# Kernel tuning notes

Measured on AMD Instinct MI355X. Metric: run time of the kernel, lower is better.

The kernel has to match this reference:

```python
import jax, jax.numpy as jnp
import numpy as np

B = 16384
D_VIS, D_LANG, D_STATE = 768, 768, 64
D = 256          # d_model
E = 4            # n_experts
K = 2            # top_k
D_IN = D_VIS + D_LANG + D_STATE
EPS = 1e-5


def layernorm(x, g, b):
    mu = x.mean(-1, keepdims=True)
    var = ((x - mu) ** 2).mean(-1, keepdims=True)
    return g * (x - mu) / jnp.sqrt(var + EPS) + b


def setup_inputs() -> dict:
    key = jax.random.key(0)
    ks = jax.random.split(key, 16)
    s = 0.02
    return {
        "vis": jax.random.normal(ks[0], (B, D_VIS), jnp.float32),
        "lang": jax.random.normal(ks[1], (B, D_LANG), jnp.float32),
        "state": jax.random.normal(ks[2], (B, D_STATE), jnp.float32),
        # fusion: Linear(d_in, d_model) + LayerNorm
        "Wf": jax.random.normal(ks[3], (D_IN, D), jnp.float32) * s,
        "bf": jnp.zeros((D,), jnp.float32),
        "gf": jnp.ones((D,), jnp.float32),
        "bfln": jnp.zeros((D,), jnp.float32),
        # gate (bias=False); random instead of zeros so routing is nontrivial
        "Wg": jax.random.normal(ks[4], (D, E), jnp.float32) * s,
        # stacked experts: Linear(d,2d) -> GELU -> Linear(2d,d) -> GELU -> Linear(d,d), then LN(x + net(x))
        "W1": jax.random.normal(ks[5], (E, D, 2 * D), jnp.float32) * s,
        "b1": jnp.zeros((E, 2 * D), jnp.float32),
        "W2": jax.random.normal(ks[6], (E, 2 * D, D), jnp.float32) * s,
        "b2": jnp.zeros((E, D), jnp.float32),
        "W3": jax.random.normal(ks[7], (E, D, D), jnp.float32) * s,
        "b3": jnp.zeros((E, D), jnp.float32),
        "eg": jnp.ones((E, D), jnp.float32),
        "eb": jnp.zeros((E, D), jnp.float32),
    }


def reference(vis, lang, state, Wf, bf, gf, bfln, Wg, W1, b1, W2, b2, W3, b3, eg, eb):
    gelu = lambda t: jax.nn.gelu(t, approximate=False)
    # fusion: Linear -> LayerNorm -> GELU  (dropout is eval-mode identity)
    x = jnp.concatenate([vis, lang, state], axis=-1) @ Wf + bf   # [B, D]
    x = gelu(layernorm(x, gf, bfln))

    logits = x @ Wg                                              # [B, E]
    all_probs = jax.nn.softmax(logits, axis=-1)
    top_vals, top_idx = jax.lax.top_k(logits, K)                 # [B, K]
    top_w = jax.nn.softmax(top_vals, axis=-1)                    # [B, K]

    # all experts densely (E small); original computes same math per masked subset
    h = gelu(jnp.einsum('bd,edh->beh', x, W1) + b1)              # [B, E, 2D]
    h = gelu(jnp.einsum('beh,ehd->bed', h, W2) + b2)             # [B, E, D]
    h = jnp.einsum('bed,edf->bef', h, W3) + b3                   # [B, E, D]
    y = layernorm(x[:, None, :] + h, eg, eb)                     # [B, E, D]

    # gather selected experts and combine with top-k weights
    y_sel = jnp.take_along_axis(y, top_idx[:, :, None], axis=1)  # [B, K, D]
    out = jnp.einsum('bk,bkd->bd', top_w, y_sel)                 # [B, D]

    # load-balance loss: importance x load
    counts = jnp.zeros((E,), x.dtype).at[top_idx.reshape(-1)].add(1.0)
    f_i = counts / (B * K)
    lb_loss = E * jnp.sum(f_i * all_probs.mean(0))
    return out, lb_loss
```

## Files before the change

kernel.cpp:

```cpp
#include <hip/hip_runtime.h>
#include <math.h>


typedef unsigned short u16;
typedef unsigned int u32;
typedef __attribute__((ext_vector_type(8))) short bf16x8;
typedef __attribute__((ext_vector_type(4))) float f32x4;

__device__ __forceinline__ float bf2f(u16 u) {
    union { u32 i; float f; } v; v.i = ((u32)u) << 16; return v.f;
}
__device__ __forceinline__ u16 f2bf(float f) {
    union { float f; u32 i; } v; v.f = f;
    u32 x = v.i;
    return (u16)((x + 0x7fffu + ((x >> 16) & 1u)) >> 16);
}
__device__ __forceinline__ float gelu_exact(float v) {
    return 0.5f * v * (1.0f + erff(v * 0.70710678118654752f));
}

typedef __attribute__((address_space(1))) void GV;
typedef __attribute__((address_space(3))) void SV;
__device__ __forceinline__ void gldlds(const void* g, void* l) {
    __builtin_amdgcn_global_load_lds((GV*)g, (SV*)l, 16, 0, 0);
}

__device__ __forceinline__ u32 pk2(u32 f0, u32 f1) {
    return __builtin_amdgcn_perm(f1, f0, 0x07060302);
}

__device__ __forceinline__ void stageA64_R32(const u16* Ag, int lda, u16* As, int tid) {
    int s = tid;
    int m = s >> 3, c = s & 7;
    gldlds(Ag + m * lda + (c ^ (m & 7)) * 8, As + s * 8);
}
__device__ __forceinline__ void stageB64(const u16* Bg, int ldb, u16* Bs, int tid) {
#pragma unroll
    for (int i = 0; i < 8; ++i) {
        int s = i * 256 + tid;
        int n = s >> 3, c = s & 7;
        gldlds(Bg + n * ldb + (c ^ (n & 7)) * 8, Bs + s * 8);
    }
}
__device__ __forceinline__ void compute64_R32(const u16* As, const u16* Bs, f32x4 acc[2][4],
                                              int w, int l16, int quad) {
#pragma unroll
    for (int ks = 0; ks < 2; ++ks) {
        bf16x8 a[2];
#pragma unroll
        for (int mt = 0; mt < 2; ++mt) {
            int m = mt * 16 + l16;
            a[mt] = *(const bf16x8*)(As + m * 64 + (((ks * 4 + quad) ^ (m & 7)) << 3));
        }
#pragma unroll
        for (int nt = 0; nt < 4; ++nt) {
            int n = w * 64 + nt * 16 + l16;
            bf16x8 b = *(const bf16x8*)(Bs + n * 64 + (((ks * 4 + quad) ^ (n & 7)) << 3));
#pragma unroll
            for (int mt = 0; mt < 2; ++mt)
                acc[mt][nt] = __builtin_amdgcn_mfma_f32_16x16x32_bf16(a[mt], b, acc[mt][nt], 0, 0, 0);
        }
    }
}
__device__ __forceinline__ void stageA128_512(const u16* Ag, int lda, u16* As, int tid) {
#pragma unroll
    for (int i = 0; i < 2; ++i) {
        int s = i * 512 + tid;
        int m = s >> 3, c = s & 7;
        gldlds(Ag + m * lda + (c ^ (m & 7)) * 8, As + s * 8);
    }
}
__device__ __forceinline__ void stageB64_512(const u16* Bg, int ldb, u16* Bs, int tid) {
#pragma unroll
    for (int i = 0; i < 4; ++i) {
        int s = i * 512 + tid;
        int n = s >> 3, c = s & 7;
        gldlds(Bg + n * ldb + (c ^ (n & 7)) * 8, Bs + s * 8);
    }
}
__device__ __forceinline__ void compute128_8w(const u16* As, const u16* Bs, f32x4 acc[4][4],
                                              int wrw, int wc, int l16, int quad) {
#pragma unroll
    for (int ks = 0; ks < 2; ++ks) {
        bf16x8 a[4];
#pragma unroll
        for (int mt = 0; mt < 4; ++mt) {
            int m = wrw * 64 + mt * 16 + l16;
            a[mt] = *(const bf16x8*)(As + m * 64 + (((ks * 4 + quad) ^ (m & 7)) << 3));
        }
#pragma unroll
        for (int nt = 0; nt < 4; ++nt) {
            int n = wc * 64 + nt * 16 + l16;
            bf16x8 b = *(const bf16x8*)(Bs + n * 64 + (((ks * 4 + quad) ^ (n & 7)) << 3));
#pragma unroll
            for (int mt = 0; mt < 4; ++mt)
                acc[mt][nt] = __builtin_amdgcn_mfma_f32_16x16x32_bf16(a[mt], b, acc[mt][nt], 0, 0, 0);
        }
    }
}

#define SEG_WF  409600
#define SEG_W1  524288
#define SEG_W2  524288
#define SEG_W3  262144
#define PREP_ITEMS (SEG_WF + SEG_W1 + SEG_W2 + SEG_W3 + 8)

__global__ __launch_bounds__(256) void prep_kernel(
    const float* __restrict__ Wf, const float* __restrict__ W1, const float* __restrict__ W2,
    const float* __restrict__ W3,
    u16* __restrict__ wft, u16* __restrict__ w1t, u16* __restrict__ w2t, u16* __restrict__ w3t,
    float* __restrict__ lbacc) {
    int idx = blockIdx.x * 256 + threadIdx.x;
    if (idx < SEG_WF) {
        int n = idx / 1600, k = idx % 1600;
        wft[idx] = f2bf(Wf[(size_t)k * 256 + n]);
        return;
    }
    idx -= SEG_WF;
    if (idx < SEG_W1) {
        int e = idx >> 17, r = idx & 131071;
        int n = r >> 8, k = r & 255;
        w1t[idx] = f2bf(W1[(size_t)e * 131072 + (size_t)k * 512 + n]);
        return;
    }
    idx -= SEG_W1;
    if (idx < SEG_W2) {
        int e = idx >> 17, r = idx & 131071;
        int n = r >> 9, k = r & 511;
        w2t[idx] = f2bf(W2[(size_t)e * 131072 + (size_t)k * 256 + n]);
        return;
    }
    idx -= SEG_W2;
    if (idx < SEG_W3) {
        int e = idx >> 16, r = idx & 65535;
        int n = r >> 8, k = r & 255;
        w3t[idx] = f2bf(W3[(size_t)e * 65536 + (size_t)k * 256 + n]);
        return;
    }
    idx -= SEG_W3;
    if (idx < 8) lbacc[idx] = 0.0f;
}

__global__ __launch_bounds__(512, 4) void fusion_kernel(
    const float* __restrict__ vis, const float* __restrict__ lang, const float* __restrict__ state,
    const u16* __restrict__ BT, const float* __restrict__ bfv_, const float* __restrict__ gf,
    const float* __restrict__ bfln, const float* __restrict__ Wg,
    u16* __restrict__ xbf, float* __restrict__ wr, float* __restrict__ lbacc) {
    __shared__ __align__(16) u32 Af[4096];
    __shared__ __align__(16) u16 Bs[16384];
    int tid = threadIdx.x;
    int w = tid >> 6, lane = tid & 63, quad = lane >> 4, l16 = lane & 15;
    int wrw = w >> 2, wc = w & 3;
    int m0 = blockIdx.x * 64;
    f32x4 acc[2][4] = {};

    for (int kit = 0; kit < 25; ++kit) {
        const float* base; int ld;
        if (kit < 12)      { base = vis   + (size_t)m0 * 768 + kit * 64;        ld = 768; }
        else if (kit < 24) { base = lang  + (size_t)m0 * 768 + (kit - 12) * 64; ld = 768; }
        else               { base = state + (size_t)m0 * 64;                    ld = 64; }
#pragma unroll
        for (int i = 0; i < 2; ++i) {
            int s = i * 512 + tid;
            int m = s >> 4, c = s & 15;
            gldlds(base + m * ld + (c ^ (m & 15)) * 4, Af + s * 4);
        }
        stageB64_512(BT + kit * 64, 1600, Bs, tid);
        __syncthreads();
#pragma unroll
        for (int ks = 0; ks < 2; ++ks) {
            bf16x8 a[2];
#pragma unroll
            for (int mt = 0; mt < 2; ++mt) {
                int m = wrw * 32 + mt * 16 + l16;
                int c0 = ks * 8 + quad * 2;
                const u32* rowp = Af + m * 64;
                uint4 f0 = *(const uint4*)(rowp + (c0 ^ (m & 15)) * 4);
                uint4 f1 = *(const uint4*)(rowp + ((c0 + 1) ^ (m & 15)) * 4);
                union { u32 u[4]; bf16x8 v; } pk;
                pk.u[0] = pk2(f0.x, f0.y); pk.u[1] = pk2(f0.z, f0.w);
                pk.u[2] = pk2(f1.x, f1.y); pk.u[3] = pk2(f1.z, f1.w);
                a[mt] = pk.v;
            }
#pragma unroll
            for (int nt = 0; nt < 4; ++nt) {
                int n = wc * 64 + nt * 16 + l16;
                bf16x8 b = *(const bf16x8*)(Bs + n * 64 + (((ks * 4 + quad) ^ (n & 7)) << 3));
#pragma unroll
                for (int mt = 0; mt < 2; ++mt)
                    acc[mt][nt] = __builtin_amdgcn_mfma_f32_16x16x32_bf16(a[mt], b, acc[mt][nt], 0, 0, 0);
            }
        }
        __syncthreads();
    }

    float2* red  = (float2*)Af;
    float*  muv  = (float*)(Af + 512);
    float*  rsv  = (float*)(Af + 576);
    float*  gred = (float*)(Af + 640);
    float*  sacc = (float*)(Af + 1664);

    float bv[4], gvv[4], blv[4]; float4 wgv[4];
#pragma unroll
    for (int nt = 0; nt < 4; ++nt) {
        int col = wc * 64 + nt * 16 + l16;
        bv[nt] = bfv_[col]; gvv[nt] = gf[col]; blv[nt] = bfln[col];
        wgv[nt] = *(const float4*)(Wg + col * 4);
    }
    if (tid < 8) sacc[tid] = 0.f;
#pragma unroll
    for (int mt = 0; mt < 2; ++mt)
#pragma unroll
        for (int r = 0; r < 4; ++r) {
            float ss = 0.f, qq = 0.f;
#pragma unroll
            for (int nt = 0; nt < 4; ++nt) {
                float v = acc[mt][nt][r] + bv[nt];
                acc[mt][nt][r] = v;
                ss += v; qq += v * v;
            }
#pragma unroll
            for (int d = 1; d < 16; d <<= 1) { ss += __shfl_xor(ss, d); qq += __shfl_xor(qq, d); }
            if (l16 == 0) red[w * 32 + mt * 16 + quad * 4 + r] = make_float2(ss, qq);
        }
    __syncthreads();
    if (tid < 64) {
        int wrh = tid >> 5, rl2 = tid & 31;
        float ss = 0.f, qq = 0.f;
#pragma unroll
        for (int ww = 0; ww < 4; ++ww) {
            float2 t = red[(wrh * 4 + ww) * 32 + rl2]; ss += t.x; qq += t.y;
        }
        float mu = ss * (1.f / 256.f);
        float var = qq * (1.f / 256.f) - mu * mu;
        muv[tid] = mu;
        rsv[tid] = 1.f / sqrtf(var + 1e-5f);
    }
    __syncthreads();
#pragma unroll
    for (int mt = 0; mt < 2; ++mt)
#pragma unroll
        for (int r = 0; r < 4; ++r) {
            int rl2 = mt * 16 + quad * 4 + r;
            int row = wrw * 32 + rl2;
            float mu = muv[row], rs = rsv[row];
#pragma unroll
            for (int nt = 0; nt < 4; ++nt) {
                int col = wc * 64 + nt * 16 + l16;
                float t = (acc[mt][nt][r] - mu) * rs * gvv[nt] + blv[nt];
                float g = gelu_exact(t);
                acc[mt][nt][r] = g;
                xbf[(size_t)(m0 + row) * 256 + col] = f2bf(g);
            }
        }
#pragma unroll
    for (int mt = 0; mt < 2; ++mt)
#pragma unroll
        for (int r = 0; r < 4; ++r) {
            int rl2 = mt * 16 + quad * 4 + r;
            float p0 = 0.f, p1 = 0.f, p2 = 0.f, p3 = 0.f;
#pragma unroll
            for (int nt = 0; nt < 4; ++nt) {
                float g = acc[mt][nt][r];
                p0 += g * wgv[nt].x; p1 += g * wgv[nt].y;
                p2 += g * wgv[nt].z; p3 += g * wgv[nt].w;
            }
#pragma unroll
            for (int d = 1; d < 16; d <<= 1) {
                p0 += __shfl_xor(p0, d); p1 += __shfl_xor(p1, d);
                p2 += __shfl_xor(p2, d); p3 += __shfl_xor(p3, d);
            }
            if (l16 == 0) {
                float* gp = gred + w * 128 + rl2 * 4;
                gp[0] = p0; gp[1] = p1; gp[2] = p2; gp[3] = p3;
            }
        }
    __syncthreads();
    if (tid < 64) {
        int row = tid, wrh = row >> 5, rl2 = row & 31;
        float lg[4];
#pragma unroll
        for (int e = 0; e < 4; ++e) {
            float s = 0.f;
#pragma unroll
            for (int ww = 0; ww < 4; ++ww) s += gred[(wrh * 4 + ww) * 128 + rl2 * 4 + e];
            lg[e] = s;
        }
        float mx = fmaxf(fmaxf(lg[0], lg[1]), fmaxf(lg[2], lg[3]));
        float ex[4]; float Z = 0.f;
#pragma unroll
        for (int e = 0; e < 4; ++e) { ex[e] = expf(lg[e] - mx); Z += ex[e]; }
        int i0 = 0; float v0 = lg[0];
#pragma unroll
        for (int e = 1; e < 4; ++e) if (lg[e] > v0) { v0 = lg[e]; i0 = e; }
        int i1 = -1; float v1 = -1e30f;
#pragma unroll
        for (int e = 0; e < 4; ++e) if (e != i0 && lg[e] > v1) { v1 = lg[e]; i1 = e; }
        float t = expf(v1 - v0);
        float wA = 1.f / (1.f + t), wB = t / (1.f + t);
        float w4[4] = {0.f, 0.f, 0.f, 0.f};
        w4[i0] = wA; w4[i1] = wB;
#pragma unroll
        for (int e = 0; e < 4; ++e) wr[(size_t)(m0 + row) * 4 + e] = w4[e];
#pragma unroll
        for (int e = 0; e < 4; ++e) atomicAdd(&sacc[e], ex[e] / Z);
        atomicAdd(&sacc[4 + i0], 1.f);
        atomicAdd(&sacc[4 + i1], 1.f);
    }
    __syncthreads();
    if (tid < 8) atomicAdd(lbacc + tid, sacc[tid]);
}

__global__ __launch_bounds__(512, 4) void expert_gemm_kernel(
    const u16* __restrict__ A, int lda, size_t aE,
    const u16* __restrict__ BT, size_t bE,
    const float* __restrict__ bias, int biasE,
    u16* __restrict__ outp, int ldo, size_t oE) {
    __shared__ __align__(16) u16 As[8192];
    __shared__ __align__(16) u16 Bs[16384];
    int tid = threadIdx.x;
    int w = tid >> 6, lane = tid & 63, quad = lane >> 4, l16 = lane & 15;
    int wrw = w >> 2, wc = w & 3;
    int m0 = blockIdx.x * 128;
    int col0 = blockIdx.y * 256;
    int e = blockIdx.z;
    f32x4 acc[4][4] = {};
    const u16* Ag = A + e * aE + (size_t)m0 * lda;
    const u16* Bg = BT + e * bE + (size_t)col0 * lda;
    int kiters = lda >> 6;
    for (int kit = 0; kit < kiters; ++kit) {
        stageA128_512(Ag + kit * 64, lda, As, tid);
        stageB64_512(Bg + kit * 64, lda, Bs, tid);
        __syncthreads();
        compute128_8w(As, Bs, acc, wrw, wc, l16, quad);
        __syncthreads();
    }
#pragma unroll
    for (int nt = 0; nt < 4; ++nt) {
        int col = col0 + wc * 64 + nt * 16 + l16;
        float bvv = bias[e * biasE + col];
#pragma unroll
        for (int mt = 0; mt < 4; ++mt)
#pragma unroll
            for (int r = 0; r < 4; ++r) {
                int row = m0 + wrw * 64 + mt * 16 + quad * 4 + r;
                outp[e * oE + (size_t)row * ldo + col] = f2bf(gelu_exact(acc[mt][nt][r] + bvv));
            }
    }
}

__global__ __launch_bounds__(256) void combine_kernel(
    const u16* __restrict__ h2, const u16* __restrict__ W3T,
    const float* __restrict__ b3, const float* __restrict__ eg, const float* __restrict__ eb,
    const u16* __restrict__ xbf, const float* __restrict__ wr,
    const float* __restrict__ lbacc, float* __restrict__ outp) {
    __shared__ __align__(16) u16 As[2048];
    __shared__ __align__(16) u16 Bs[16384];
    __shared__ __align__(16) u16 xs[8192];
    __shared__ float wl[128];
    int tid = threadIdx.x;
    int w = tid >> 6, lane = tid & 63, quad = lane >> 4, l16 = lane & 15;
    int m0 = blockIdx.x * 32;
    if (blockIdx.x == 0 && tid == 0) {
        float lb = 0.f;
#pragma unroll
        for (int e = 0; e < 4; ++e)
            lb += (lbacc[4 + e] / 32768.f) * (lbacc[e] / 16384.f);
        outp[4194304] = 4.f * lb;
    }
#pragma unroll
    for (int i = 0; i < 4; ++i) {
        int s = i * 256 + tid;
        *(uint4*)(xs + s * 8) = *(const uint4*)(xbf + (size_t)m0 * 256 + s * 8);
    }
    if (tid < 128) wl[tid] = wr[(size_t)m0 * 4 + tid];
    float2* red = (float2*)As;
    float* muv = (float*)((char*)As + 1024);
    float* rsv = (float*)((char*)As + 1152);
    f32x4 oacc[2][4] = {};
    for (int e = 0; e < 4; ++e) {
        __syncthreads();
        f32x4 acc[2][4] = {};
        const u16* Ag = h2 + ((size_t)e * 16384 + m0) * 256;
        const u16* Bg = W3T + (size_t)e * 65536;
        for (int kit = 0; kit < 4; ++kit) {
            stageA64_R32(Ag + kit * 64, 256, As, tid);
            stageB64(Bg + kit * 64, 256, Bs, tid);
            __syncthreads();
            compute64_R32(As, Bs, acc, w, l16, quad);
            __syncthreads();
        }
        float b3v[4], egv[4], ebv[4];
#pragma unroll
        for (int nt = 0; nt < 4; ++nt) {
            int col = w * 64 + nt * 16 + l16;
            b3v[nt] = b3[e * 256 + col]; egv[nt] = eg[e * 256 + col]; ebv[nt] = eb[e * 256 + col];
        }
#pragma unroll
        for (int mt = 0; mt < 2; ++mt)
#pragma unroll
            for (int r = 0; r < 4; ++r) {
                int rl = mt * 16 + quad * 4 + r;
                float ss = 0.f, qq = 0.f;
#pragma unroll
                for (int nt = 0; nt < 4; ++nt) {
                    int col = w * 64 + nt * 16 + l16;
                    float v = acc[mt][nt][r] + b3v[nt] + bf2f(xs[rl * 256 + col]);
                    acc[mt][nt][r] = v;
                    ss += v; qq += v * v;
                }
#pragma unroll
                for (int d = 1; d < 16; d <<= 1) { ss += __shfl_xor(ss, d); qq += __shfl_xor(qq, d); }
                if (l16 == 0) red[w * 32 + rl] = make_float2(ss, qq);
            }
        __syncthreads();
        if (tid < 32) {
            float ss = 0.f, qq = 0.f;
#pragma unroll
            for (int ww = 0; ww < 4; ++ww) { float2 t = red[ww * 32 + tid]; ss += t.x; qq += t.y; }
            float mu = ss * (1.f / 256.f);
            float var = qq * (1.f / 256.f) - mu * mu;
            muv[tid] = mu;
            rsv[tid] = 1.f / sqrtf(var + 1e-5f);
        }
        __syncthreads();
#pragma unroll
        for (int mt = 0; mt < 2; ++mt)
#pragma unroll
            for (int r = 0; r < 4; ++r) {
                int rl = mt * 16 + quad * 4 + r;
                float mu = muv[rl], rs = rsv[rl], we = wl[rl * 4 + e];
#pragma unroll
                for (int nt = 0; nt < 4; ++nt) {
                    float y = (acc[mt][nt][r] - mu) * rs * egv[nt] + ebv[nt];
                    oacc[mt][nt][r] += we * y;
                }
            }
    }
#pragma unroll
    for (int mt = 0; mt < 2; ++mt)
#pragma unroll
        for (int r = 0; r < 4; ++r) {
            int rl = mt * 16 + quad * 4 + r;
#pragma unroll
            for (int nt = 0; nt < 4; ++nt) {
                int col = w * 64 + nt * 16 + l16;
                outp[(size_t)(m0 + rl) * 256 + col] = oacc[mt][nt][r];
            }
        }
}

extern "C" void kernel_launch(void* const* d_in, const int* in_sizes, int n_in,
                              void* d_out, int out_size, void* d_ws, size_t ws_size,
                              hipStream_t stream) {
    const float* vis   = (const float*)d_in[0];
    const float* lang  = (const float*)d_in[1];
    const float* state = (const float*)d_in[2];
    const float* Wf    = (const float*)d_in[3];
    const float* bf_   = (const float*)d_in[4];
    const float* gf    = (const float*)d_in[5];
    const float* bfln  = (const float*)d_in[6];
    const float* Wg    = (const float*)d_in[7];
    const float* W1    = (const float*)d_in[8];
    const float* b1    = (const float*)d_in[9];
    const float* W2    = (const float*)d_in[10];
    const float* b2    = (const float*)d_in[11];
    const float* W3    = (const float*)d_in[12];
    const float* b3    = (const float*)d_in[13];
    const float* eg    = (const float*)d_in[14];
    const float* eb    = (const float*)d_in[15];
    float* outp = (float*)d_out;

    char* ws = (char*)d_ws;
    size_t off = 0;
    float* lbacc = (float*)(ws + off); off += 256;
    u16* WFT  = (u16*)(ws + off); off += 819200UL;
    u16* W1T  = (u16*)(ws + off); off += 1048576UL;
    u16* W2T  = (u16*)(ws + off); off += 1048576UL;
    u16* W3T  = (u16*)(ws + off); off += 524288UL;
    u16* XBF  = (u16*)(ws + off); off += 8388608UL;
    float* WR = (float*)(ws + off); off += 262144UL;
    u16* H1   = (u16*)(ws + off); off += 67108864UL;
    u16* H2   = (u16*)(ws + off); off += 33554432UL;
    if (ws_size < off) return;

    int prep_blocks = (PREP_ITEMS + 255) / 256;
    prep_kernel<<<prep_blocks, 256, 0, stream>>>(Wf, W1, W2, W3, WFT, W1T, W2T, W3T, lbacc);
    fusion_kernel<<<256, 512, 0, stream>>>(vis, lang, state, WFT, bf_, gf, bfln, Wg,
                                           XBF, WR, lbacc);
    expert_gemm_kernel<<<dim3(128, 2, 4), 512, 0, stream>>>(
        XBF, 256, 0, W1T, 131072, b1, 512, H1, 512, 8388608UL);
    expert_gemm_kernel<<<dim3(128, 1, 4), 512, 0, stream>>>(
        H1, 512, 8388608UL, W2T, 131072, b2, 256, H2, 256, 4194304UL);
    combine_kernel<<<512, 256, 0, stream>>>(H2, W3T, b3, eg, eb, XBF, WR, lbacc, outp);
}
```

Measured before the change: 319.1 us.

## Tile weight transpose via LDS, retile fusion and combine kernels

The prep kernel now transposes weights through a padded 32x32 shared-memory tile, so both the fp32 reads and the bf16 writes are coalesced instead of strided reads per element. The fusion kernel moves from 64-row to 32-row blocks with eight warps splitting the 256 columns, doubling the grid to 512 blocks for more parallelism. The combine kernel goes from 32-row to 64-row tiles, so each W3 tile staged in LDS is reused across twice as many rows. The trade-offs are more accumulator registers and LDS in combine, and in fusion the weight tile is reloaded for half as many rows per block.

```diff
diff --git a/kernel.cpp b/kernel.cpp
--- a/kernel.cpp
+++ b/kernel.cpp
@@ -29,10 +29,13 @@
     return __builtin_amdgcn_perm(f1, f0, 0x07060302);
 }
 
-__device__ __forceinline__ void stageA64_R32(const u16* Ag, int lda, u16* As, int tid) {
-    int s = tid;
-    int m = s >> 3, c = s & 7;
-    gldlds(Ag + m * lda + (c ^ (m & 7)) * 8, As + s * 8);
+__device__ __forceinline__ void stageA64(const u16* Ag, int lda, u16* As, int tid) {
+#pragma unroll
+    for (int i = 0; i < 2; ++i) {
+        int s = i * 256 + tid;
+        int m = s >> 3, c = s & 7;
+        gldlds(Ag + m * lda + (c ^ (m & 7)) * 8, As + s * 8);
+    }
 }
 __device__ __forceinline__ void stageB64(const u16* Bg, int ldb, u16* Bs, int tid) {
 #pragma unroll
@@ -42,13 +45,13 @@
         gldlds(Bg + n * ldb + (c ^ (n & 7)) * 8, Bs + s * 8);
     }
 }
-__device__ __forceinline__ void compute64_R32(const u16* As, const u16* Bs, f32x4 acc[2][4],
-                                              int w, int l16, int quad) {
+__device__ __forceinline__ void compute64(const u16* As, const u16* Bs, f32x4 acc[4][4],
+                                          int w, int l16, int quad) {
 #pragma unroll
     for (int ks = 0; ks < 2; ++ks) {
-        bf16x8 a[2];
-#pragma unroll
-        for (int mt = 0; mt < 2; ++mt) {
+        bf16x8 a[4];
+#pragma unroll
+        for (int mt = 0; mt < 4; ++mt) {
             int m = mt * 16 + l16;
             a[mt] = *(const bf16x8*)(As + m * 64 + (((ks * 4 + quad) ^ (m & 7)) << 3));
         }
@@ -57,7 +60,7 @@
             int n = w * 64 + nt * 16 + l16;
             bf16x8 b = *(const bf16x8*)(Bs + n * 64 + (((ks * 4 + quad) ^ (n & 7)) << 3));
 #pragma unroll
-            for (int mt = 0; mt < 2; ++mt)
+            for (int mt = 0; mt < 4; ++mt)
                 acc[mt][nt] = __builtin_amdgcn_mfma_f32_16x16x32_bf16(a[mt], b, acc[mt][nt], 0, 0, 0);
         }
     }
@@ -98,47 +101,36 @@
         }
     }
 }
-
-#define SEG_WF  409600
-#define SEG_W1  524288
-#define SEG_W2  524288
-#define SEG_W3  262144
-#define PREP_ITEMS (SEG_WF + SEG_W1 + SEG_W2 + SEG_W3 + 8)
 
 __global__ __launch_bounds__(256) void prep_kernel(
     const float* __restrict__ Wf, const float* __restrict__ W1, const float* __restrict__ W2,
     const float* __restrict__ W3,
     u16* __restrict__ wft, u16* __restrict__ w1t, u16* __restrict__ w2t, u16* __restrict__ w3t,
     float* __restrict__ lbacc) {
-    int idx = blockIdx.x * 256 + threadIdx.x;
-    if (idx < SEG_WF) {
-        int n = idx / 1600, k = idx % 1600;
-        wft[idx] = f2bf(Wf[(size_t)k * 256 + n]);
-        return;
-    }
-    idx -= SEG_WF;
-    if (idx < SEG_W1) {
-        int e = idx >> 17, r = idx & 131071;
-        int n = r >> 8, k = r & 255;
-        w1t[idx] = f2bf(W1[(size_t)e * 131072 + (size_t)k * 512 + n]);
-        return;
-    }
-    idx -= SEG_W1;
-    if (idx < SEG_W2) {
-        int e = idx >> 17, r = idx & 131071;
-        int n = r >> 9, k = r & 511;
-        w2t[idx] = f2bf(W2[(size_t)e * 131072 + (size_t)k * 256 + n]);
-        return;
-    }
-    idx -= SEG_W2;
-    if (idx < SEG_W3) {
-        int e = idx >> 16, r = idx & 65535;
-        int n = r >> 8, k = r & 255;
-        w3t[idx] = f2bf(W3[(size_t)e * 65536 + (size_t)k * 256 + n]);
-        return;
-    }
-    idx -= SEG_W3;
-    if (idx < 8) lbacc[idx] = 0.0f;
+    int b = blockIdx.x;
+    int tid = threadIdx.x;
+    const float* src; u16* dst; int K, N, kt, ntl;
+    if (b < 400)      { src = Wf; dst = wft; K = 1600; N = 256; kt = b % 50; ntl = b / 50; }
+    else if (b < 912) { int r = b - 400, e = r >> 7; r &= 127;
+                        src = W1 + (size_t)e * 131072; dst = w1t + (size_t)e * 131072;
+                        K = 256; N = 512; kt = r & 7; ntl = r >> 3; }
+    else if (b < 1424){ int r = b - 912, e = r >> 7; r &= 127;
+                        src = W2 + (size_t)e * 131072; dst = w2t + (size_t)e * 131072;
+                        K = 512; N = 256; kt = r & 15; ntl = r >> 4; }
+    else if (b < 1680){ int r = b - 1424, e = r >> 6; r &= 63;
+                        src = W3 + (size_t)e * 65536; dst = w3t + (size_t)e * 65536;
+                        K = 256; N = 256; kt = r & 7; ntl = r >> 3; }
+    else { if (tid < 8) lbacc[tid] = 0.0f; return; }
+    int k0 = kt * 32, n0 = ntl * 32;
+    __shared__ float tl[32][33];
+    int j = tid & 31, i0 = (tid >> 5) << 2;
+#pragma unroll
+    for (int ii = 0; ii < 4; ++ii)
+        tl[i0 + ii][j] = src[(size_t)(k0 + i0 + ii) * N + n0 + j];
+    __syncthreads();
+#pragma unroll
+    for (int ii = 0; ii < 4; ++ii)
+        dst[(size_t)(n0 + i0 + ii) * K + k0 + j] = f2bf(tl[j][i0 + ii]);
 }
 
 __global__ __launch_bounds__(512, 4) void fusion_kernel(
@@ -146,22 +138,20 @@
     const u16* __restrict__ BT, const float* __restrict__ bfv_, const float* __restrict__ gf,
     const float* __restrict__ bfln, const float* __restrict__ Wg,
     u16* __restrict__ xbf, float* __restrict__ wr, float* __restrict__ lbacc) {
-    __shared__ __align__(16) u32 Af[4096];
+    __shared__ __align__(16) u32 Af[2048];
     __shared__ __align__(16) u16 Bs[16384];
     int tid = threadIdx.x;
     int w = tid >> 6, lane = tid & 63, quad = lane >> 4, l16 = lane & 15;
-    int wrw = w >> 2, wc = w & 3;
-    int m0 = blockIdx.x * 64;
-    f32x4 acc[2][4] = {};
+    int m0 = blockIdx.x * 32;
+    f32x4 acc[2][2] = {};
 
     for (int kit = 0; kit < 25; ++kit) {
         const float* base; int ld;
         if (kit < 12)      { base = vis   + (size_t)m0 * 768 + kit * 64;        ld = 768; }
         else if (kit < 24) { base = lang  + (size_t)m0 * 768 + (kit - 12) * 64; ld = 768; }
         else               { base = state + (size_t)m0 * 64;                    ld = 64; }
-#pragma unroll
-        for (int i = 0; i < 2; ++i) {
-            int s = i * 512 + tid;
+        {
+            int s = tid;
             int m = s >> 4, c = s & 15;
             gldlds(base + m * ld + (c ^ (m & 15)) * 4, Af + s * 4);
         }
@@ -172,7 +162,7 @@
             bf16x8 a[2];
 #pragma unroll
             for (int mt = 0; mt < 2; ++mt) {
-                int m = wrw * 32 + mt * 16 + l16;
+                int m = mt * 16 + l16;
                 int c0 = ks * 8 + quad * 2;
                 const u32* rowp = Af + m * 64;
                 uint4 f0 = *(const uint4*)(rowp + (c0 ^ (m & 15)) * 4);
@@ -183,8 +173,8 @@
                 a[mt] = pk.v;
             }
 #pragma unroll
-            for (int nt = 0; nt < 4; ++nt) {
-                int n = wc * 64 + nt * 16 + l16;
+            for (int nt = 0; nt < 2; ++nt) {
+                int n = w * 32 + nt * 16 + l16;
                 bf16x8 b = *(const bf16x8*)(Bs + n * 64 + (((ks * 4 + quad) ^ (n & 7)) << 3));
 #pragma unroll
                 for (int mt = 0; mt < 2; ++mt)
@@ -196,14 +186,14 @@
 
     float2* red  = (float2*)Af;
     float*  muv  = (float*)(Af + 512);
-    float*  rsv  = (float*)(Af + 576);
-    float*  gred = (float*)(Af + 640);
-    float*  sacc = (float*)(Af + 1664);
-
-    float bv[4], gvv[4], blv[4]; float4 wgv[4];
-#pragma unroll
-    for (int nt = 0; nt < 4; ++nt) {
-        int col = wc * 64 + nt * 16 + l16;
+    float*  rsv  = (float*)(Af + 544);
+    float*  gred = (float*)(Af + 576);
+    float*  sacc = (float*)(Af + 1600);
+
+    float bv[2], gvv[2], blv[2]; float4 wgv[2];
+#pragma unroll
+    for (int nt = 0; nt < 2; ++nt) {
+        int col = w * 32 + nt * 16 + l16;
         bv[nt] = bfv_[col]; gvv[nt] = gf[col]; blv[nt] = bfln[col];
         wgv[nt] = *(const float4*)(Wg + col * 4);
     }
@@ -214,7 +204,7 @@
         for (int r = 0; r < 4; ++r) {
             float ss = 0.f, qq = 0.f;
 #pragma unroll
-            for (int nt = 0; nt < 4; ++nt) {
+            for (int nt = 0; nt < 2; ++nt) {
                 float v = acc[mt][nt][r] + bv[nt];
                 acc[mt][nt][r] = v;
                 ss += v; qq += v * v;
@@ -224,13 +214,10 @@
             if (l16 == 0) red[w * 32 + mt * 16 + quad * 4 + r] = make_float2(ss, qq);
         }
     __syncthreads();
-    if (tid < 64) {
-        int wrh = tid >> 5, rl2 = tid & 31;
+    if (tid < 32) {
         float ss = 0.f, qq = 0.f;
 #pragma unroll
-        for (int ww = 0; ww < 4; ++ww) {
-            float2 t = red[(wrh * 4 + ww) * 32 + rl2]; ss += t.x; qq += t.y;
-        }
+        for (int ww = 0; ww < 8; ++ww) { float2 t = red[ww * 32 + tid]; ss += t.x; qq += t.y; }
         float mu = ss * (1.f / 256.f);
         float var = qq * (1.f / 256.f) - mu * mu;
         muv[tid] = mu;
@@ -241,26 +228,25 @@
     for (int mt = 0; mt < 2; ++mt)
 #pragma unroll
         for (int r = 0; r < 4; ++r) {
-            int rl2 = mt * 16 + quad * 4 + r;
-            int row = wrw * 32 + rl2;
-            float mu = muv[row], rs = rsv[row];
-#pragma unroll
-            for (int nt = 0; nt < 4; ++nt) {
-                int col = wc * 64 + nt * 16 + l16;
+            int rl = mt * 16 + quad * 4 + r;
+            float mu = muv[rl], rs = rsv[rl];
+#pragma unroll
+            for (int nt = 0; nt < 2; ++nt) {
+                int col = w * 32 + nt * 16 + l16;
                 float t = (acc[mt][nt][r] - mu) * rs * gvv[nt] + blv[nt];
                 float g = gelu_exact(t);
                 acc[mt][nt][r] = g;
-                xbf[(size_t)(m0 + row) * 256 + col] = f2bf(g);
+                xbf[(size_t)(m0 + rl) * 256 + col] = f2bf(g);
             }
         }
 #pragma unroll
     for (int mt = 0; mt < 2; ++mt)
 #pragma unroll
         for (int r = 0; r < 4; ++r) {
-            int rl2 = mt * 16 + quad * 4 + r;
+            int rl = mt * 16 + quad * 4 + r;
             float p0 = 0.f, p1 = 0.f, p2 = 0.f, p3 = 0.f;
 #pragma unroll
-            for (int nt = 0; nt < 4; ++nt) {
+            for (int nt = 0; nt < 2; ++nt) {
                 float g = acc[mt][nt][r];
                 p0 += g * wgv[nt].x; p1 += g * wgv[nt].y;
                 p2 += g * wgv[nt].z; p3 += g * wgv[nt].w;
@@ -271,19 +257,19 @@
                 p2 += __shfl_xor(p2, d); p3 += __shfl_xor(p3, d);
             }
             if (l16 == 0) {
-                float* gp = gred + w * 128 + rl2 * 4;
+                float* gp = gred + w * 128 + rl * 4;
                 gp[0] = p0; gp[1] = p1; gp[2] = p2; gp[3] = p3;
             }
         }
     __syncthreads();
-    if (tid < 64) {
-        int row = tid, wrh = row >> 5, rl2 = row & 31;
+    if (tid < 32) {
+        int row = tid;
         float lg[4];
 #pragma unroll
         for (int e = 0; e < 4; ++e) {
             float s = 0.f;
 #pragma unroll
-            for (int ww = 0; ww < 4; ++ww) s += gred[(wrh * 4 + ww) * 128 + rl2 * 4 + e];
+            for (int ww = 0; ww < 8; ++ww) s += gred[ww * 128 + row * 4 + e];
             lg[e] = s;
         }
         float mx = fmaxf(fmaxf(lg[0], lg[1]), fmaxf(lg[2], lg[3]));
@@ -354,13 +340,15 @@
     const float* __restrict__ b3, const float* __restrict__ eg, const float* __restrict__ eb,
     const u16* __restrict__ xbf, const float* __restrict__ wr,
     const float* __restrict__ lbacc, float* __restrict__ outp) {
-    __shared__ __align__(16) u16 As[2048];
+    __shared__ __align__(16) u16 As[4096];
     __shared__ __align__(16) u16 Bs[16384];
-    __shared__ __align__(16) u16 xs[8192];
-    __shared__ float wl[128];
+    __shared__ __align__(16) u16 xs[16384];
+    __shared__ float wl[256];
+    __shared__ float2 red[256];
+    __shared__ float muv[64], rsv[64];
     int tid = threadIdx.x;
     int w = tid >> 6, lane = tid & 63, quad = lane >> 4, l16 = lane & 15;
-    int m0 = blockIdx.x * 32;
+    int m0 = blockIdx.x * 64;
     if (blockIdx.x == 0 && tid == 0) {
         float lb = 0.f;
 #pragma unroll
@@ -369,25 +357,22 @@
         outp[4194304] = 4.f * lb;
     }
 #pragma unroll
-    for (int i = 0; i < 4; ++i) {
+    for (int i = 0; i < 8; ++i) {
         int s = i * 256 + tid;
         *(uint4*)(xs + s * 8) = *(const uint4*)(xbf + (size_t)m0 * 256 + s * 8);
     }
-    if (tid < 128) wl[tid] = wr[(size_t)m0 * 4 + tid];
-    float2* red = (float2*)As;
-    float* muv = (float*)((char*)As + 1024);
-    float* rsv = (float*)((char*)As + 1152);
-    f32x4 oacc[2][4] = {};
+    wl[tid] = wr[(size_t)m0 * 4 + tid];
+    f32x4 oacc[4][4] = {};
     for (int e = 0; e < 4; ++e) {
         __syncthreads();
-        f32x4 acc[2][4] = {};
+        f32x4 acc[4][4] = {};
         const u16* Ag = h2 + ((size_t)e * 16384 + m0) * 256;
         const u16* Bg = W3T + (size_t)e * 65536;
         for (int kit = 0; kit < 4; ++kit) {
-            stageA64_R32(Ag + kit * 64, 256, As, tid);
+            stageA64(Ag + kit * 64, 256, As, tid);
             stageB64(Bg + kit * 64, 256, Bs, tid);
             __syncthreads();
-            compute64_R32(As, Bs, acc, w, l16, quad);
+            compute64(As, Bs, acc, w, l16, quad);
             __syncthreads();
         }
         float b3v[4], egv[4], ebv[4];
@@ -397,27 +382,27 @@
             b3v[nt] = b3[e * 256 + col]; egv[nt] = eg[e * 256 + col]; ebv[nt] = eb[e * 256 + col];
         }
 #pragma unroll
-        for (int mt = 0; mt < 2; ++mt)
+        for (int mt = 0; mt < 4; ++mt)
 #pragma unroll
             for (int r = 0; r < 4; ++r) {
-                int rl = mt * 16 + quad * 4 + r;
+                int row = mt * 16 + quad * 4 + r;
                 float ss = 0.f, qq = 0.f;
 #pragma unroll
                 for (int nt = 0; nt < 4; ++nt) {
                     int col = w * 64 + nt * 16 + l16;
-                    float v = acc[mt][nt][r] + b3v[nt] + bf2f(xs[rl * 256 + col]);
+                    float v = acc[mt][nt][r] + b3v[nt] + bf2f(xs[row * 256 + col]);
                     acc[mt][nt][r] = v;
                     ss += v; qq += v * v;
                 }
 #pragma unroll
                 for (int d = 1; d < 16; d <<= 1) { ss += __shfl_xor(ss, d); qq += __shfl_xor(qq, d); }
-                if (l16 == 0) red[w * 32 + rl] = make_float2(ss, qq);
-            }
-        __syncthreads();
-        if (tid < 32) {
+                if (l16 == 0) red[w * 64 + row] = make_float2(ss, qq);
+            }
+        __syncthreads();
+        if (tid < 64) {
             float ss = 0.f, qq = 0.f;
 #pragma unroll
-            for (int ww = 0; ww < 4; ++ww) { float2 t = red[ww * 32 + tid]; ss += t.x; qq += t.y; }
+            for (int ww = 0; ww < 4; ++ww) { float2 t = red[ww * 64 + tid]; ss += t.x; qq += t.y; }
             float mu = ss * (1.f / 256.f);
             float var = qq * (1.f / 256.f) - mu * mu;
             muv[tid] = mu;
@@ -425,11 +410,11 @@
         }
         __syncthreads();
 #pragma unroll
-        for (int mt = 0; mt < 2; ++mt)
+        for (int mt = 0; mt < 4; ++mt)
 #pragma unroll
             for (int r = 0; r < 4; ++r) {
-                int rl = mt * 16 + quad * 4 + r;
-                float mu = muv[rl], rs = rsv[rl], we = wl[rl * 4 + e];
+                int row = mt * 16 + quad * 4 + r;
+                float mu = muv[row], rs = rsv[row], we = wl[row * 4 + e];
 #pragma unroll
                 for (int nt = 0; nt < 4; ++nt) {
                     float y = (acc[mt][nt][r] - mu) * rs * egv[nt] + ebv[nt];
@@ -438,14 +423,14 @@
             }
     }
 #pragma unroll
-    for (int mt = 0; mt < 2; ++mt)
+    for (int mt = 0; mt < 4; ++mt)
 #pragma unroll
         for (int r = 0; r < 4; ++r) {
-            int rl = mt * 16 + quad * 4 + r;
+            int row = mt * 16 + quad * 4 + r;
 #pragma unroll
             for (int nt = 0; nt < 4; ++nt) {
                 int col = w * 64 + nt * 16 + l16;
-                outp[(size_t)(m0 + rl) * 256 + col] = oacc[mt][nt][r];
+                outp[(size_t)(m0 + row) * 256 + col] = oacc[mt][nt][r];
             }
         }
 }
@@ -484,13 +469,12 @@
     u16* H2   = (u16*)(ws + off); off += 33554432UL;
     if (ws_size < off) return;
 
-    int prep_blocks = (PREP_ITEMS + 255) / 256;
-    prep_kernel<<<prep_blocks, 256, 0, stream>>>(Wf, W1, W2, W3, WFT, W1T, W2T, W3T, lbacc);
-    fusion_kernel<<<256, 512, 0, stream>>>(vis, lang, state, WFT, bf_, gf, bfln, Wg,
+    prep_kernel<<<1681, 256, 0, stream>>>(Wf, W1, W2, W3, WFT, W1T, W2T, W3T, lbacc);
+    fusion_kernel<<<512, 512, 0, stream>>>(vis, lang, state, WFT, bf_, gf, bfln, Wg,
                                            XBF, WR, lbacc);
     expert_gemm_kernel<<<dim3(128, 2, 4), 512, 0, stream>>>(
         XBF, 256, 0, W1T, 131072, b1, 512, H1, 512, 8388608UL);
     expert_gemm_kernel<<<dim3(128, 1, 4), 512, 0, stream>>>(
         H1, 512, 8388608UL, W2T, 131072, b2, 256, H2, 256, 4194304UL);
-    combine_kernel<<<512, 256, 0, stream>>>(H2, W3T, b3, eg, eb, XBF, WR, lbacc, outp);
-}
+    combine_kernel<<<256, 256, 0, stream>>>(H2, W3T, b3, eg, eb, XBF, WR, lbacc, outp);
+}
```

Result: no change. 319.6 us (+0.2%).
